# Optimization experiments

Hardware: AMD Instinct MI355X
Metric: run time of the kernel (lower is better)

Reference implementation:

```python
import math
import jax, jax.numpy as jnp
import numpy as np

B, S, D = 4, 2048, 1024
N_HEAD = 16


def setup_inputs() -> dict:
    key = jax.random.key(0)
    k1, k2 = jax.random.split(key)
    x = jax.random.normal(k1, (B, S, D), dtype=jnp.float32)
    # xavier-uniform style scale for the fused QKV kernel
    limit = math.sqrt(6.0 / (D + 3 * D))
    W_qkv = jax.random.uniform(k2, (D, 3 * D), dtype=jnp.float32, minval=-limit, maxval=limit)
    b_qkv = jnp.zeros((3 * D,), dtype=jnp.float32)
    return {"x": x, "W_qkv": W_qkv, "b_qkv": b_qkv}


def reference(x, W_qkv, b_qkv):
    batch_size, seq_len, d_model = x.shape
    head_dim = d_model // N_HEAD
    # fused QKV projection: [B, S, 3D]
    qkv = jnp.einsum('bsd,de->bse', x, W_qkv) + b_qkv
    qkv = qkv.reshape(batch_size, seq_len, N_HEAD, 3 * head_dim)
    qkv = qkv.transpose(0, 2, 1, 3)  # [B, H, S, 3*hd]
    q, k, v = jnp.split(qkv, 3, axis=-1)
    # scaled dot-product attention with causal mask
    attn_logits = jnp.einsum('bhqd,bhkd->bhqk', q, k) / math.sqrt(head_dim)
    causal = jnp.tril(jnp.ones((seq_len, seq_len), dtype=jnp.float32))[None, None]
    attn_logits = jnp.where(causal == 0, -jnp.inf, attn_logits)
    attn = jax.nn.softmax(attn_logits, axis=-1)
    out = jnp.einsum('bhqk,bhkd->bhqd', attn, v)  # [B, H, S, hd]
    out = out.transpose(0, 2, 1, 3).reshape(batch_size, seq_len, -1)
    return out
```

## Files before the change

### kernel.cpp

```cpp
#include <hip/hip_runtime.h>
#include <hip/hip_bf16.h>
#include <cstdint>

typedef __bf16 bf16x8 __attribute__((ext_vector_type(8)));
typedef float f32x4 __attribute__((ext_vector_type(4)));
typedef float f32x16 __attribute__((ext_vector_type(16)));

__device__ inline unsigned short f2bf(float f) {
    union { float f; unsigned int u; } v; v.f = f;
    unsigned int u = v.u;
    unsigned int r = (u + 0x7FFFu + ((u >> 16) & 1u)) >> 16;
    return (unsigned short)r;
}

__device__ inline f32x4 mfma16(bf16x8 a, bf16x8 b, f32x4 c) {
    return __builtin_amdgcn_mfma_f32_16x16x32_bf16(a, b, c, 0, 0, 0);
}

__device__ inline f32x16 mfma32(bf16x8 a, bf16x8 b, f32x16 c) {
    return __builtin_amdgcn_mfma_f32_32x32x16_bf16(a, b, c, 0, 0, 0);
}

__device__ inline bf16x8 ldfrag(const unsigned short* p) {
    uint4 v = *(const uint4*)p;
    return __builtin_bit_cast(bf16x8, v);
}

__device__ inline void cp16(const unsigned short* g, unsigned short* l) {
    __builtin_amdgcn_global_load_lds(
        (const __attribute__((address_space(1))) unsigned int*)g,
        (__attribute__((address_space(3))) unsigned int*)l,
        16, 0, 0);
}

__device__ inline unsigned int pkbf(float a, float b) {
    return __builtin_amdgcn_perm(__builtin_bit_cast(unsigned int, b),
                                 __builtin_bit_cast(unsigned int, a),
                                 0x07060302u);
}

__device__ inline void plswap(unsigned int& a, unsigned int& b) {
    typedef unsigned int u32x2 __attribute__((ext_vector_type(2)));
    u32x2 r = __builtin_amdgcn_permlane32_swap(a, b, false, false);
    a = r[0]; b = r[1];
}

__global__ __launch_bounds__(256) void k_prep(
    const float* __restrict__ x, unsigned short* __restrict__ xbf,
    const float* __restrict__ W, unsigned short* __restrict__ Wt) {
    __shared__ float tile[32][33];
    if (blockIdx.x < 8192) {
        int i = blockIdx.x * 256 + threadIdx.x;
        float4 f = ((const float4*)x)[i];
        ushort4 o;
        o.x = f2bf(f.x); o.y = f2bf(f.y); o.z = f2bf(f.z); o.w = f2bf(f.w);
        ((ushort4*)xbf)[i] = o;
    } else {
        int bid = blockIdx.x - 8192;
        int nt = bid % 96, kt = bid / 96;
        int tx = threadIdx.x & 31, ty = threadIdx.x >> 5;
#pragma unroll
        for (int yy = 0; yy < 4; ++yy) {
            int y = ty + yy * 8;
            tile[y][tx] = W[(size_t)(kt * 32 + y) * 3072 + nt * 32 + tx];
        }
        __syncthreads();
#pragma unroll
        for (int yy = 0; yy < 4; ++yy) {
            int nrow = ty + yy * 8;
            Wt[(size_t)(nt * 32 + nrow) * 1024 + kt * 32 + tx] =
                f2bf(tile[tx][nrow]);
        }
    }
}

__global__ __launch_bounds__(256, 2) void k_qkv_gemm(
    const unsigned short* __restrict__ A,
    const unsigned short* __restrict__ Bt,
    const float* __restrict__ bias,
    unsigned short* __restrict__ C) {
    __shared__ __align__(16) unsigned short As[2 * 128 * 64];
    __shared__ __align__(16) unsigned short Bs[2 * 192 * 64];
    const int tid = threadIdx.x;
    const int lane = tid & 63;
    const int w = tid >> 6;
    const int wm = w >> 1, wn = w & 1;
    const int l31 = lane & 31;
    const int hi = lane >> 5;
    const int xr7 = l31 & 7;
    const int m0 = blockIdx.y * 128;
    const int n0 = blockIdx.x * 192;

    const int srow = tid >> 3, sseg = tid & 7;
    const int gsw = (sseg ^ (srow & 7)) * 8;
    const unsigned short* pA = A + (size_t)(m0 + srow) * 1024 + gsw;
    const unsigned short* pB = Bt + (size_t)(n0 + srow) * 1024 + gsw;

    f32x16 acc[2][3] = {};

    auto stage = [&](int buf, int k0) {
        unsigned short* da = &As[buf * 8192 + tid * 8];
        unsigned short* db = &Bs[buf * 12288 + tid * 8];
#pragma unroll
        for (int i = 0; i < 4; ++i)
            cp16(pA + (size_t)i * 32 * 1024 + k0, da + i * 2048);
#pragma unroll
        for (int j = 0; j < 6; ++j)
            cp16(pB + (size_t)j * 32 * 1024 + k0, db + j * 2048);
    };

    stage(0, 0);
    asm volatile("s_waitcnt vmcnt(0)" ::: "memory");
    __builtin_amdgcn_s_barrier();

    for (int kt = 0; kt < 16; ++kt) {
        const int buf = kt & 1;
        if (kt < 15) stage(buf ^ 1, (kt + 1) * 64);

        const unsigned short* ab = &As[buf * 8192];
        const unsigned short* bb = &Bs[buf * 12288];
        bf16x8 af[2][4], bfr[3][4];
#pragma unroll
        for (int rb = 0; rb < 2; ++rb) {
            const int r = wm * 64 + rb * 32 + l31;
#pragma unroll
            for (int ks = 0; ks < 4; ++ks)
                af[rb][ks] = ldfrag(ab + r * 64 + ((ks * 2 + hi) ^ xr7) * 8);
        }
#pragma unroll
        for (int cb = 0; cb < 3; ++cb) {
            const int r = wn * 96 + cb * 32 + l31;
#pragma unroll
            for (int ks = 0; ks < 4; ++ks)
                bfr[cb][ks] = ldfrag(bb + r * 64 + ((ks * 2 + hi) ^ xr7) * 8);
        }
#pragma unroll
        for (int rb = 0; rb < 2; ++rb)
#pragma unroll
            for (int cb = 0; cb < 3; ++cb)
#pragma unroll
                for (int ks = 0; ks < 4; ++ks)
                    acc[rb][cb] = mfma32(af[rb][ks], bfr[cb][ks], acc[rb][cb]);

        asm volatile("s_waitcnt vmcnt(0)" ::: "memory");
        __builtin_amdgcn_s_barrier();
    }

#pragma unroll
    for (int cb = 0; cb < 3; ++cb) {
        const int col = n0 + wn * 96 + cb * 32 + l31;
        const float bv = bias[col];
#pragma unroll
        for (int rb = 0; rb < 2; ++rb) {
            const int rbase = m0 + wm * 64 + rb * 32 + 4 * hi;
#pragma unroll
            for (int g = 0; g < 4; ++g)
#pragma unroll
                for (int rr = 0; rr < 4; ++rr) {
                    const int row = rbase + g * 8 + rr;
                    C[(size_t)row * 3072 + col] =
                        f2bf(acc[rb][cb][g * 4 + rr] + bv);
                }
        }
    }
}

__global__ __launch_bounds__(256) void k_transpose_v(
    const unsigned short* __restrict__ qkv,
    unsigned short* __restrict__ VtG) {
    __shared__ unsigned short t[64][65];
    const int st = blockIdx.x;
    const int h = blockIdx.y;
    const int b = blockIdx.z;
    const int tid = threadIdx.x;
    const int voff = h * 192 + 128;
    const size_t base = (size_t)b * 2048 * 3072;
#pragma unroll
    for (int i = 0; i < 2; ++i) {
        int c = tid + i * 256;
        int row = c >> 3, seg = c & 7;
        uint4 v = *(const uint4*)(qkv + base + (size_t)(st * 64 + row) * 3072 + voff + seg * 8);
        unsigned short u8[8];
        *(uint4*)u8 = v;
#pragma unroll
        for (int u = 0; u < 8; ++u) t[row][seg * 8 + u] = u8[u];
    }
    __syncthreads();
    const size_t obase = ((size_t)(b * 16 + h) * 64) * 2048 + st * 64;
#pragma unroll
    for (int i = 0; i < 2; ++i) {
        int c = tid + i * 256;
        int drow = c >> 3, seg = c & 7;
        unsigned short u8[8];
#pragma unroll
        for (int u = 0; u < 8; ++u) u8[u] = t[seg * 8 + u][drow];
        *(uint4*)(VtG + obase + (size_t)drow * 2048 + seg * 8) = *(uint4*)u8;
    }
}

__global__ __launch_bounds__(256) void k_attn(
    const unsigned short* __restrict__ qkv,
    const unsigned short* __restrict__ VtG,
    float* __restrict__ out) {
    const int p = blockIdx.x;
    const int hb = p & 63;
    const int h = hb & 15;
    const int b = hb >> 4;
    const int qt = 31 - (p >> 6);
    const int tid = threadIdx.x;
    const int lane = tid & 63;
    const int w = tid >> 6;
    const int wm = w >> 1;
    const int wn = w & 1;
    const int l31 = lane & 31;
    const int hi = lane >> 5;

    __shared__ __align__(16) unsigned short KsF[2 * 64 * 64];
    __shared__ __align__(16) unsigned short VsF[2 * 64 * 64];

    const size_t base = (size_t)b * 2048 * 3072;
    const int qoff = h * 192, koff = h * 192 + 64;
    const size_t vtbase = (size_t)(b * 16 + h) * 64 * 2048;

    const int srow0 = tid >> 3, sseg = tid & 7;
    const int gsw = (sseg ^ (srow0 & 7)) * 8;
    unsigned short* kd0 = &KsF[tid * 8];
    unsigned short* kd1 = &KsF[2048 + tid * 8];
    unsigned short* vd0 = &VsF[tid * 8];
    unsigned short* vd1 = &VsF[2048 + tid * 8];

    const int xr7 = l31 & 7;
    const int kfbase = (32 * wm + l31) * 64;
    const int vfb0 = l31 * 64;
    const int vfb1 = (32 + l31) * 64;
    const int qcol = 32 * wn + l31;

    const float sc = 0.125f * 1.44269504088896340736f;

    const int qrow = qt * 64 + qcol;
    const unsigned short* qp = qkv + base + (size_t)qrow * 3072 + qoff + hi * 8;
    bf16x8 bq[4];
#pragma unroll
    for (int t = 0; t < 4; ++t) bq[t] = ldfrag(qp + t * 16);

    const unsigned short* kp0 = qkv + base + koff + (size_t)srow0 * 3072 + gsw;
    const unsigned short* kp1 = kp0 + (size_t)32 * 3072;
    const unsigned short* vp0 = VtG + vtbase + (size_t)srow0 * 2048 + gsw;
    const unsigned short* vp1 = vp0 + (size_t)32 * 2048;

    f32x16 acc0 = {0,0,0,0,0,0,0,0,0,0,0,0,0,0,0,0};
    f32x16 acc1 = {0,0,0,0,0,0,0,0,0,0,0,0,0,0,0,0};
    float ptot = 0.f;

    cp16(kp0, kd0); cp16(kp1, kd1); cp16(vp0, vd0); cp16(vp1, vd1);
    __syncthreads();

    for (int kt = 0; kt <= qt; ++kt) {
        const int bo = (kt & 1) * 4096;
        const int bn = bo ^ 4096;
        if (kt < qt) {
            kp0 += 64 * 3072; kp1 += 64 * 3072;
            vp0 += 64;        vp1 += 64;
            cp16(kp0, kd0 + bn); cp16(kp1, kd1 + bn);
            cp16(vp0, vd0 + bn); cp16(vp1, vd1 + bn);
        }

        f32x16 s = {0,0,0,0,0,0,0,0,0,0,0,0,0,0,0,0};
#pragma unroll
        for (int t = 0; t < 4; ++t) {
            const unsigned short* ka =
                &KsF[bo + kfbase + ((2 * t + hi) ^ xr7) * 8];
            s = mfma32(ldfrag(ka), bq[t], s);
        }

        if (kt == qt) {
#pragma unroll
            for (int r = 0; r < 16; ++r) {
                const int srow = 32 * wm + (r & 3) + 8 * (r >> 2) + 4 * hi;
                if (srow > qcol) s[r] = -3.0e38f;
            }
        }

        float pvv[16];
#pragma unroll
        for (int r = 0; r < 16; ++r) {
            pvv[r] = __builtin_amdgcn_exp2f(
                __builtin_fmaf(s[r], sc, -16.0f));
            ptot += pvv[r];
        }
        unsigned int pk0 = pkbf(pvv[0], pvv[1]),   pk1 = pkbf(pvv[2], pvv[3]);
        unsigned int pk2 = pkbf(pvv[4], pvv[5]),   pk3 = pkbf(pvv[6], pvv[7]);
        unsigned int pk4 = pkbf(pvv[8], pvv[9]),   pk5 = pkbf(pvv[10], pvv[11]);
        unsigned int pk6 = pkbf(pvv[12], pvv[13]), pk7 = pkbf(pvv[14], pvv[15]);
        plswap(pk0, pk2); plswap(pk1, pk3);
        plswap(pk4, pk6); plswap(pk5, pk7);
        uint4 w0; w0.x = pk0; w0.y = pk1; w0.z = pk2; w0.w = pk3;
        uint4 w1; w1.x = pk4; w1.y = pk5; w1.z = pk6; w1.w = pk7;
        const bf16x8 pf0 = __builtin_bit_cast(bf16x8, w0);
        const bf16x8 pf1 = __builtin_bit_cast(bf16x8, w1);

        const int su0 = ((4 * wm + hi) ^ xr7) * 8;
        const int su1 = ((4 * wm + 2 + hi) ^ xr7) * 8;
        acc0 = mfma32(ldfrag(&VsF[bo + vfb0 + su0]), pf0, acc0);
        acc0 = mfma32(ldfrag(&VsF[bo + vfb0 + su1]), pf1, acc0);
        acc1 = mfma32(ldfrag(&VsF[bo + vfb1 + su0]), pf0, acc1);
        acc1 = mfma32(ldfrag(&VsF[bo + vfb1 + su1]), pf1, acc1);

        __syncthreads();
    }

    float* Sc = (float*)KsF;
    float* Pt = (float*)VsF;
    const int lb = (wn * 64 + lane) * 8;
    if (wm == 1) {
#pragma unroll
        for (int g = 0; g < 4; ++g) {
            float4 v;
            v.x = acc0[g * 4 + 0]; v.y = acc0[g * 4 + 1];
            v.z = acc0[g * 4 + 2]; v.w = acc0[g * 4 + 3];
            ((float4*)Sc)[lb + (g ^ (lane & 7))] = v;
        }
#pragma unroll
        for (int g = 0; g < 4; ++g) {
            float4 v;
            v.x = acc1[g * 4 + 0]; v.y = acc1[g * 4 + 1];
            v.z = acc1[g * 4 + 2]; v.w = acc1[g * 4 + 3];
            ((float4*)Sc)[lb + ((g + 4) ^ (lane & 7))] = v;
        }
        Pt[wn * 64 + lane] = ptot;
    }
    __syncthreads();
    if (wm == 0) {
#pragma unroll
        for (int g = 0; g < 4; ++g) {
            float4 v = ((const float4*)Sc)[lb + (g ^ (lane & 7))];
            acc0[g * 4 + 0] += v.x; acc0[g * 4 + 1] += v.y;
            acc0[g * 4 + 2] += v.z; acc0[g * 4 + 3] += v.w;
        }
#pragma unroll
        for (int g = 0; g < 4; ++g) {
            float4 v = ((const float4*)Sc)[lb + ((g + 4) ^ (lane & 7))];
            acc1[g * 4 + 0] += v.x; acc1[g * 4 + 1] += v.y;
            acc1[g * 4 + 2] += v.z; acc1[g * 4 + 3] += v.w;
        }
        float l = ptot + Pt[wn * 64 + lane];
        l += __shfl_xor(l, 32, 64);
        const float inv = __builtin_amdgcn_rcpf(l);
        float* op = out + ((size_t)b * 2048 + qrow) * 1024 + h * 64 + 4 * hi;
#pragma unroll
        for (int g = 0; g < 4; ++g) {
            float4 v;
            v.x = acc0[g * 4 + 0] * inv; v.y = acc0[g * 4 + 1] * inv;
            v.z = acc0[g * 4 + 2] * inv; v.w = acc0[g * 4 + 3] * inv;
            *(float4*)(op + g * 8) = v;
        }
#pragma unroll
        for (int g = 0; g < 4; ++g) {
            float4 v;
            v.x = acc1[g * 4 + 0] * inv; v.y = acc1[g * 4 + 1] * inv;
            v.z = acc1[g * 4 + 2] * inv; v.w = acc1[g * 4 + 3] * inv;
            *(float4*)(op + 32 + g * 8) = v;
        }
    }
}

extern "C" void kernel_launch(void* const* d_in, const int* in_sizes, int n_in,
                              void* d_out, int out_size, void* d_ws, size_t ws_size,
                              hipStream_t stream) {
    const float* x = (const float*)d_in[0];
    const float* W = (const float*)d_in[1];
    const float* bq = (const float*)d_in[2];
    float* out = (float*)d_out;

    unsigned short* xbf = (unsigned short*)d_ws;
    unsigned short* wtbf = xbf + (size_t)8192 * 1024;
    unsigned short* qkvbf = wtbf + (size_t)3072 * 1024;
    unsigned short* VtG = xbf;

    k_prep<<<8192 + 3072, 256, 0, stream>>>(x, xbf, W, wtbf);
    k_qkv_gemm<<<dim3(16, 64), 256, 0, stream>>>(xbf, wtbf, bq, qkvbf);
    k_transpose_v<<<dim3(32, 16, 4), 256, 0, stream>>>(qkvbf, VtG);
    k_attn<<<2048, 256, 0, stream>>>(qkvbf, VtG, out);
}
```

Baseline: 218.9 us.

## Fuse V transpose into QKV GEMM epilogue and triple-buffer K loop

The QKV GEMM epilogue now writes the V part of each head directly in a transposed, blocked layout inside the qkv buffer, so the separate V-transpose kernel launch and its extra global round trip are removed. The attention kernel reads V from that in-place transposed region. The GEMM main loop also changes from a K-step of 64 with double buffering and full drains to a K-step of 32 with a three-stage ring and partial vmcnt waits, so loads overlap compute more deeply. The epilogue now does scattered 8-byte stores for V, and the smaller K-step doubles the number of barriers.

```diff
diff --git a/kernel.cpp b/kernel.cpp
--- a/kernel.cpp
+++ b/kernel.cpp
@@ -3,7 +3,6 @@
 #include <cstdint>
 
 typedef __bf16 bf16x8 __attribute__((ext_vector_type(8)));
-typedef float f32x4 __attribute__((ext_vector_type(4)));
 typedef float f32x16 __attribute__((ext_vector_type(16)));
 
 __device__ inline unsigned short f2bf(float f) {
@@ -11,10 +10,6 @@
     unsigned int u = v.u;
     unsigned int r = (u + 0x7FFFu + ((u >> 16) & 1u)) >> 16;
     return (unsigned short)r;
-}
-
-__device__ inline f32x4 mfma16(bf16x8 a, bf16x8 b, f32x4 c) {
-    return __builtin_amdgcn_mfma_f32_16x16x32_bf16(a, b, c, 0, 0, 0);
 }
 
 __device__ inline f32x16 mfma32(bf16x8 a, bf16x8 b, f32x16 c) {
@@ -79,128 +74,119 @@
     const unsigned short* __restrict__ Bt,
     const float* __restrict__ bias,
     unsigned short* __restrict__ C) {
-    __shared__ __align__(16) unsigned short As[2 * 128 * 64];
-    __shared__ __align__(16) unsigned short Bs[2 * 192 * 64];
+    __shared__ __align__(16) unsigned short As[3 * 128 * 32];
+    __shared__ __align__(16) unsigned short Bs[3 * 192 * 32];
     const int tid = threadIdx.x;
     const int lane = tid & 63;
     const int w = tid >> 6;
     const int wm = w >> 1, wn = w & 1;
     const int l31 = lane & 31;
     const int hi = lane >> 5;
-    const int xr7 = l31 & 7;
+    const int xr3 = l31 & 3;
+    const int h = blockIdx.x;
+    const int n0 = h * 192;
     const int m0 = blockIdx.y * 128;
-    const int n0 = blockIdx.x * 192;
-
-    const int srow = tid >> 3, sseg = tid & 7;
-    const int gsw = (sseg ^ (srow & 7)) * 8;
+    const int b = blockIdx.y >> 4;
+
+    const int srow = tid >> 2, sseg = tid & 3;
+    const int gsw = (sseg ^ (srow & 3)) * 8;
     const unsigned short* pA = A + (size_t)(m0 + srow) * 1024 + gsw;
     const unsigned short* pB = Bt + (size_t)(n0 + srow) * 1024 + gsw;
 
     f32x16 acc[2][3] = {};
 
     auto stage = [&](int buf, int k0) {
-        unsigned short* da = &As[buf * 8192 + tid * 8];
-        unsigned short* db = &Bs[buf * 12288 + tid * 8];
-#pragma unroll
-        for (int i = 0; i < 4; ++i)
-            cp16(pA + (size_t)i * 32 * 1024 + k0, da + i * 2048);
-#pragma unroll
-        for (int j = 0; j < 6; ++j)
-            cp16(pB + (size_t)j * 32 * 1024 + k0, db + j * 2048);
+        unsigned short* da = &As[buf * 4096 + tid * 8];
+        unsigned short* db = &Bs[buf * 6144 + tid * 8];
+        cp16(pA + k0, da);
+        cp16(pA + 64 * 1024 + k0, da + 2048);
+        cp16(pB + k0, db);
+        cp16(pB + 64 * 1024 + k0, db + 2048);
+        cp16(pB + 128 * 1024 + k0, db + 4096);
     };
 
     stage(0, 0);
-    asm volatile("s_waitcnt vmcnt(0)" ::: "memory");
-    __builtin_amdgcn_s_barrier();
-
-    for (int kt = 0; kt < 16; ++kt) {
-        const int buf = kt & 1;
-        if (kt < 15) stage(buf ^ 1, (kt + 1) * 64);
-
-        const unsigned short* ab = &As[buf * 8192];
-        const unsigned short* bb = &Bs[buf * 12288];
-        bf16x8 af[2][4], bfr[3][4];
+    stage(1, 32);
+
+    int buf = 0, nbuf = 2;
+    for (int kt = 0; kt < 32; ++kt) {
+        if (kt == 31)
+            asm volatile("s_waitcnt vmcnt(0)" ::: "memory");
+        else
+            asm volatile("s_waitcnt vmcnt(5)" ::: "memory");
+        __builtin_amdgcn_s_barrier();
+        if (kt < 30) {
+            stage(nbuf, (kt + 2) * 32);
+            nbuf = (nbuf == 2) ? 0 : nbuf + 1;
+        }
+
+        const unsigned short* ab = &As[buf * 4096];
+        const unsigned short* bb = &Bs[buf * 6144];
+        bf16x8 af[2][2], bfr[3][2];
 #pragma unroll
         for (int rb = 0; rb < 2; ++rb) {
             const int r = wm * 64 + rb * 32 + l31;
 #pragma unroll
-            for (int ks = 0; ks < 4; ++ks)
-                af[rb][ks] = ldfrag(ab + r * 64 + ((ks * 2 + hi) ^ xr7) * 8);
+            for (int ks = 0; ks < 2; ++ks)
+                af[rb][ks] = ldfrag(ab + r * 32 + ((ks * 2 + hi) ^ xr3) * 8);
         }
 #pragma unroll
         for (int cb = 0; cb < 3; ++cb) {
             const int r = wn * 96 + cb * 32 + l31;
 #pragma unroll
-            for (int ks = 0; ks < 4; ++ks)
-                bfr[cb][ks] = ldfrag(bb + r * 64 + ((ks * 2 + hi) ^ xr7) * 8);
+            for (int ks = 0; ks < 2; ++ks)
+                bfr[cb][ks] = ldfrag(bb + r * 32 + ((ks * 2 + hi) ^ xr3) * 8);
         }
 #pragma unroll
         for (int rb = 0; rb < 2; ++rb)
 #pragma unroll
             for (int cb = 0; cb < 3; ++cb)
 #pragma unroll
-                for (int ks = 0; ks < 4; ++ks)
+                for (int ks = 0; ks < 2; ++ks)
                     acc[rb][cb] = mfma32(af[rb][ks], bfr[cb][ks], acc[rb][cb]);
 
-        asm volatile("s_waitcnt vmcnt(0)" ::: "memory");
-        __builtin_amdgcn_s_barrier();
-    }
-
+        asm volatile("s_waitcnt lgkmcnt(0)" ::: "memory");
+        buf = (buf == 2) ? 0 : buf + 1;
+    }
+
+    const size_t cbase = (size_t)b * 2048 * 3072;
 #pragma unroll
     for (int cb = 0; cb < 3; ++cb) {
-        const int col = n0 + wn * 96 + cb * 32 + l31;
+        const int colw = wn * 96 + cb * 32;
+        const int col = n0 + colw + l31;
         const float bv = bias[col];
 #pragma unroll
         for (int rb = 0; rb < 2; ++rb) {
             const int rbase = m0 + wm * 64 + rb * 32 + 4 * hi;
-#pragma unroll
-            for (int g = 0; g < 4; ++g)
-#pragma unroll
-                for (int rr = 0; rr < 4; ++rr) {
-                    const int row = rbase + g * 8 + rr;
-                    C[(size_t)row * 3072 + col] =
-                        f2bf(acc[rb][cb][g * 4 + rr] + bv);
+            if (wn == 1 && cb >= 1) {
+                const int d = colw - 128 + l31;
+#pragma unroll
+                for (int g = 0; g < 4; ++g) {
+                    const int s0 = (rbase + g * 8) & 2047;
+                    unsigned int lo = (unsigned int)f2bf(acc[rb][cb][g * 4 + 0] + bv) |
+                                      ((unsigned int)f2bf(acc[rb][cb][g * 4 + 1] + bv) << 16);
+                    unsigned int hi2 = (unsigned int)f2bf(acc[rb][cb][g * 4 + 2] + bv) |
+                                       ((unsigned int)f2bf(acc[rb][cb][g * 4 + 3] + bv) << 16);
+                    uint2 pk; pk.x = lo; pk.y = hi2;
+                    *(uint2*)(C + cbase + (size_t)(d * 32 + (s0 >> 6)) * 3072 +
+                              n0 + 128 + (s0 & 63)) = pk;
                 }
-        }
-    }
-}
-
-__global__ __launch_bounds__(256) void k_transpose_v(
-    const unsigned short* __restrict__ qkv,
-    unsigned short* __restrict__ VtG) {
-    __shared__ unsigned short t[64][65];
-    const int st = blockIdx.x;
-    const int h = blockIdx.y;
-    const int b = blockIdx.z;
-    const int tid = threadIdx.x;
-    const int voff = h * 192 + 128;
-    const size_t base = (size_t)b * 2048 * 3072;
-#pragma unroll
-    for (int i = 0; i < 2; ++i) {
-        int c = tid + i * 256;
-        int row = c >> 3, seg = c & 7;
-        uint4 v = *(const uint4*)(qkv + base + (size_t)(st * 64 + row) * 3072 + voff + seg * 8);
-        unsigned short u8[8];
-        *(uint4*)u8 = v;
-#pragma unroll
-        for (int u = 0; u < 8; ++u) t[row][seg * 8 + u] = u8[u];
-    }
-    __syncthreads();
-    const size_t obase = ((size_t)(b * 16 + h) * 64) * 2048 + st * 64;
-#pragma unroll
-    for (int i = 0; i < 2; ++i) {
-        int c = tid + i * 256;
-        int drow = c >> 3, seg = c & 7;
-        unsigned short u8[8];
-#pragma unroll
-        for (int u = 0; u < 8; ++u) u8[u] = t[seg * 8 + u][drow];
-        *(uint4*)(VtG + obase + (size_t)drow * 2048 + seg * 8) = *(uint4*)u8;
+            } else {
+#pragma unroll
+                for (int g = 0; g < 4; ++g)
+#pragma unroll
+                    for (int rr = 0; rr < 4; ++rr) {
+                        const int row = rbase + g * 8 + rr;
+                        C[(size_t)row * 3072 + col] =
+                            f2bf(acc[rb][cb][g * 4 + rr] + bv);
+                    }
+            }
+        }
     }
 }
 
 __global__ __launch_bounds__(256) void k_attn(
     const unsigned short* __restrict__ qkv,
-    const unsigned short* __restrict__ VtG,
     float* __restrict__ out) {
     const int p = blockIdx.x;
     const int hb = p & 63;
@@ -219,8 +205,7 @@
     __shared__ __align__(16) unsigned short VsF[2 * 64 * 64];
 
     const size_t base = (size_t)b * 2048 * 3072;
-    const int qoff = h * 192, koff = h * 192 + 64;
-    const size_t vtbase = (size_t)(b * 16 + h) * 64 * 2048;
+    const int qoff = h * 192, koff = h * 192 + 64, voff = h * 192 + 128;
 
     const int srow0 = tid >> 3, sseg = tid & 7;
     const int gsw = (sseg ^ (srow0 & 7)) * 8;
@@ -245,8 +230,8 @@
 
     const unsigned short* kp0 = qkv + base + koff + (size_t)srow0 * 3072 + gsw;
     const unsigned short* kp1 = kp0 + (size_t)32 * 3072;
-    const unsigned short* vp0 = VtG + vtbase + (size_t)srow0 * 2048 + gsw;
-    const unsigned short* vp1 = vp0 + (size_t)32 * 2048;
+    const unsigned short* vp0 = qkv + base + (size_t)(srow0 * 32) * 3072 + voff + gsw;
+    const unsigned short* vp1 = vp0 + (size_t)1024 * 3072;
 
     f32x16 acc0 = {0,0,0,0,0,0,0,0,0,0,0,0,0,0,0,0};
     f32x16 acc1 = {0,0,0,0,0,0,0,0,0,0,0,0,0,0,0,0};
@@ -260,7 +245,7 @@
         const int bn = bo ^ 4096;
         if (kt < qt) {
             kp0 += 64 * 3072; kp1 += 64 * 3072;
-            vp0 += 64;        vp1 += 64;
+            vp0 += 3072;      vp1 += 3072;
             cp16(kp0, kd0 + bn); cp16(kp1, kd1 + bn);
             cp16(vp0, vd0 + bn); cp16(vp1, vd1 + bn);
         }
@@ -375,10 +360,8 @@
     unsigned short* xbf = (unsigned short*)d_ws;
     unsigned short* wtbf = xbf + (size_t)8192 * 1024;
     unsigned short* qkvbf = wtbf + (size_t)3072 * 1024;
-    unsigned short* VtG = xbf;
 
     k_prep<<<8192 + 3072, 256, 0, stream>>>(x, xbf, W, wtbf);
     k_qkv_gemm<<<dim3(16, 64), 256, 0, stream>>>(xbf, wtbf, bq, qkvbf);
-    k_transpose_v<<<dim3(32, 16, 4), 256, 0, stream>>>(qkvbf, VtG);
-    k_attn<<<2048, 256, 0, stream>>>(qkvbf, VtG, out);
-}
+    k_attn<<<2048, 256, 0, stream>>>(qkvbf, out);
+}
```

New measurement: 225.0 us. 2.8% more time.
